# Optimization experiments

Measured on AMD Instinct MI355X. Metric: run time of the kernel, lower is better.

Reference implementation:

```python
import jax, jax.numpy as jnp
import numpy as np

N, E, L = 50000, 800000, 200000
IN_FEATS, HID = 256, 128
EPS = 1e-5


def setup_inputs() -> dict:
    key = jax.random.key(0)
    ks = jax.random.split(key, 32)
    def lin(k, fan_in, fan_out):
        s = 1.0 / np.sqrt(fan_in)
        return jax.random.uniform(k, (fan_out, fan_in), jnp.float32, -s, s)
    inp = {
        "x": jax.random.normal(ks[0], (N, IN_FEATS), jnp.float32),
        "edge_index": jax.random.randint(ks[1], (2, E), 0, N, jnp.int32),
        "edge_label_index": jax.random.randint(ks[2], (2, L), 0, N, jnp.int32),
        # SAGEConv layers: lin_l (on aggregated neighbors, with bias), lin_r (root, no bias)
        "w1l": lin(ks[3], IN_FEATS, HID), "b1l": jnp.zeros((HID,), jnp.float32), "w1r": lin(ks[4], IN_FEATS, HID),
        "w2l": lin(ks[5], HID, HID), "b2l": jnp.zeros((HID,), jnp.float32), "w2r": lin(ks[6], HID, HID),
        "w3l": lin(ks[7], HID, HID), "b3l": jnp.zeros((HID,), jnp.float32), "w3r": lin(ks[8], HID, HID),
        # BatchNorm (eval mode: running stats)
        "bn1_g": jnp.ones((HID,), jnp.float32), "bn1_b": jnp.zeros((HID,), jnp.float32),
        "bn1_m": 0.1 * jax.random.normal(ks[9], (HID,), jnp.float32),
        "bn1_v": jax.random.uniform(ks[10], (HID,), jnp.float32, 0.5, 1.5),
        "bn2_g": jnp.ones((HID,), jnp.float32), "bn2_b": jnp.zeros((HID,), jnp.float32),
        "bn2_m": 0.1 * jax.random.normal(ks[11], (HID,), jnp.float32),
        "bn2_v": jax.random.uniform(ks[12], (HID,), jnp.float32, 0.5, 1.5),
        # Decoder MLP
        "dw1": lin(ks[13], 2 * HID, HID), "db1": jnp.zeros((HID,), jnp.float32),
        "dw2": lin(ks[14], HID, 1), "db2": jnp.zeros((1,), jnp.float32),
    }
    return inp


def _sage_conv(x, src, dst, wl, bl, wr):
    # mean-aggregate neighbor features at dst, then lin_l(agg) + lin_r(x)
    n = x.shape[0]
    agg = jax.ops.segment_sum(x[src], dst, num_segments=n)
    cnt = jax.ops.segment_sum(jnp.ones_like(dst, dtype=x.dtype), dst, num_segments=n)
    mean = agg / jnp.maximum(cnt, 1.0)[:, None]
    return mean @ wl.T + bl + x @ wr.T


def _bn_eval(h, g, b, m, v):
    return (h - m) * (g * jax.lax.rsqrt(v + EPS)) + b


def reference(x, edge_index, edge_label_index,
              w1l, b1l, w1r, w2l, b2l, w2r, w3l, b3l, w3r,
              bn1_g, bn1_b, bn1_m, bn1_v, bn2_g, bn2_b, bn2_m, bn2_v,
              dw1, db1, dw2, db2):
    src, dst = edge_index[0], edge_index[1]
    h = _sage_conv(x, src, dst, w1l, b1l, w1r)
    h = jax.nn.relu(_bn_eval(h, bn1_g, bn1_b, bn1_m, bn1_v))
    h = _sage_conv(h, src, dst, w2l, b2l, w2r)
    h = jax.nn.relu(_bn_eval(h, bn2_g, bn2_b, bn2_m, bn2_v))
    z = _sage_conv(h, src, dst, w3l, b3l, w3r)
    # decode: gather pair embeddings, concat, MLP -> scalar per pair
    s, d = edge_label_index[0], edge_label_index[1]
    pair = jnp.concatenate([z[s], z[d]], axis=1)  # [L, 2*HID]
    hdec = jax.nn.relu(pair @ dw1.T + db1)
    return (hdec @ dw2.T + db2).reshape(-1)
```

## Files before the change

### kernel.cpp

```cpp
#include <hip/hip_runtime.h>
#include <hip/hip_fp16.h>


typedef unsigned int uint;
using s16x8 = __attribute__((ext_vector_type(8))) short;
using f32x4 = __attribute__((ext_vector_type(4))) float;

__device__ inline void bsplit(float v, ushort& hi, ushort& lo) {
    uint u = __float_as_uint(v);
    uint hb = (u + 0x7FFFu + ((u >> 16) & 1u)) >> 16;
    hi = (ushort)hb;
    float r = v - __uint_as_float(hb << 16);
    uint u2 = __float_as_uint(r);
    lo = (ushort)((u2 + 0x7FFFu + ((u2 >> 16) & 1u)) >> 16);
}

__device__ inline ushort f2h(float v) { return __half_as_ushort(__float2half(v)); }

__device__ inline float4 h4f(uint2 r) {
    float2 fa = __half22float2(*(const __half2*)&r.x);
    float2 fb = __half22float2(*(const __half2*)&r.y);
    return make_float4(fa.x, fa.y, fb.x, fb.y);
}

__device__ inline uint swz(uint i, uint r) {
    return (i & ~63u) | ((i ^ (r << 3)) & 56u) | (i & 7u);
}

__device__ inline void gload16(const void* g, void* l) {
    __builtin_amdgcn_global_load_lds(
        (const __attribute__((address_space(1))) unsigned int*)g,
        (__attribute__((address_space(3))) unsigned int*)l, 16, 0, 0);
}

__global__ __launch_bounds__(256) void prep_kernel(
    const float* __restrict__ x, ushort* __restrict__ A3, int totalconv, int nconv,
    const int* __restrict__ dst, int* __restrict__ cnt, int* __restrict__ rank,
    int E, int ncount,
    const float* __restrict__ w1l, const float* __restrict__ w1r,
    const float* __restrict__ w2l, const float* __restrict__ w2r,
    const float* __restrict__ w3l, const float* __restrict__ w3r,
    const float* __restrict__ dw1,
    ushort* __restrict__ WS1, ushort* __restrict__ WS2,
    ushort* __restrict__ WS3, ushort* __restrict__ WS4)
{
    const int g = blockIdx.x >> 4;
    const int r16 = blockIdx.x & 15;
    if (r16 < 12) {
        int ci = g * 12 + r16;
        if (ci >= nconv) return;
        int e = ci * 256 + threadIdx.x;
        if (e >= totalconv) return;
        uint row = e >> 6;
        uint k4 = (e & 63) << 2;
        float4 v = *(const float4*)(x + (size_t)row * 256 + k4);
        ushort4 hi, lo;
        bsplit(v.x, hi.x, lo.x); bsplit(v.y, hi.y, lo.y);
        bsplit(v.z, hi.z, lo.z); bsplit(v.w, hi.w, lo.w);
        ushort* d = A3 + (size_t)row * 512;
        *(ushort4*)(d + swz(k4, row))       = hi;
        *(ushort4*)(d + swz(k4 + 256, row)) = lo;
    } else if (r16 < 15) {
        int qi = g * 3 + (r16 - 12);
        if (qi >= ncount) return;
        int i = qi * 256 + threadIdx.x;
        if (i < E) rank[i] = atomicAdd(&cnt[dst[i]], 1);
    } else {
        int w = g;
        if (w >= 1024) return;
        uint n = w & 255;
        int which = w >> 8;
        uint k = threadIdx.x;
        const float *wa, *wb;
        uint K, lda, aoff, boff;
        ushort* WS;
        switch (which) {
            case 0:  wa = w1l; wb = w1r; K = 256; lda = 256; aoff = 0; boff = 0;   WS = WS1; break;
            case 1:  wa = w2l; wb = w2r; K = 128; lda = 128; aoff = 0; boff = 0;   WS = WS2; break;
            case 2:  wa = w3l; wb = w3r; K = 128; lda = 128; aoff = 0; boff = 0;   WS = WS3; break;
            default: wa = dw1; wb = dw1; K = 128; lda = 256; aoff = 0; boff = 128; WS = WS4; break;
        }
        if (k >= K) return;
        const float* srcr = (n < 128) ? (wa + (size_t)n * lda + aoff)
                                      : (wb + (size_t)(n - 128) * lda + boff);
        ushort hi, lo;
        bsplit(srcr[k], hi, lo);
        ushort* d = WS + (size_t)n * 3 * K;
        d[swz(k, n)]         = hi;
        d[swz(K + k, n)]     = lo;
        d[swz(2 * K + k, n)] = hi;
    }
}

__global__ void scanA_kernel(const int* __restrict__ cnt, int* __restrict__ ptr,
                             int* __restrict__ tilesum, int n) {
    __shared__ int sd[1024];
    int t = threadIdx.x;
    int i = blockIdx.x * 1024 + t;
    int v = (i < n) ? cnt[i] : 0;
    sd[t] = v;
    __syncthreads();
    #pragma unroll
    for (int off = 1; off < 1024; off <<= 1) {
        int add = (t >= off) ? sd[t - off] : 0;
        __syncthreads();
        sd[t] += add;
        __syncthreads();
    }
    if (i < n) ptr[i] = sd[t] - v;
    if (t == 1023) tilesum[blockIdx.x] = sd[t];
}

__global__ void scanC_kernel(int* __restrict__ ptr, const int* __restrict__ tilesum,
                             int n, int ntiles) {
    int i = blockIdx.x * 256 + threadIdx.x;
    int t = i >> 10;
    int base = 0;
    for (int b = 0; b < t; ++b) base += tilesum[b];
    if (i < n) ptr[i] += base;
    if (i == 0) {
        int tot = 0;
        for (int b = 0; b < ntiles; ++b) tot += tilesum[b];
        ptr[n] = tot;
    }
}

__global__ void scatter_kernel(const int* __restrict__ src, const int* __restrict__ dst,
                               const int* __restrict__ ptr, const int* __restrict__ rank,
                               int* __restrict__ edges, int E) {
    int i = blockIdx.x * blockDim.x + threadIdx.x;
    if (i < E) edges[ptr[dst[i]] + rank[i]] = src[i];
}

template <int KP, int CRF16>
__global__ __launch_bounds__(256, 2) void mm_kernel(const ushort* __restrict__ A,
                                                    const ushort* __restrict__ WS,
                                                    ushort* __restrict__ Cl,
                                                    void* __restrict__ Cr_, int M) {
    constexpr int KS  = (KP / 64) + (KP / 128);
    constexpr int WKP = KP + KP / 2;
    __shared__ ushort At[128 * 64];
    __shared__ ushort Bt[256 * 64];
    const int t = threadIdx.x;
    const int lane = t & 63;
    const int wave = t >> 6;
    const int wm = wave >> 1, wn = wave & 1;
    const int row0 = blockIdx.x * 128;
    const int l15 = lane & 15;
    const int l4 = lane >> 4;
    const int l8 = lane >> 3;
    const int c8 = lane & 7;

    f32x4 acc[4][8] = {};

    for (int s = 0; s < KS; ++s) {
        const int as = (s < KP / 128) ? s : s - (KP / 128);
        #pragma unroll
        for (int j = 0; j < 4; ++j) {
            int jj = wave + j * 4;
            int r = jj * 8 + l8;
            gload16(A + (size_t)(row0 + r) * KP + as * 64 + c8 * 8,
                    (char*)At + jj * 1024 + lane * 16);
        }
        #pragma unroll
        for (int j = 0; j < 8; ++j) {
            int jj = wave + j * 4;
            int r = jj * 8 + l8;
            gload16(WS + (size_t)r * WKP + s * 64 + c8 * 8,
                    (char*)Bt + jj * 1024 + lane * 16);
        }
        __syncthreads();
        #pragma unroll
        for (int kk = 0; kk < 64; kk += 32) {
            s16x8 af[4], bf[8];
            #pragma unroll
            for (int mi = 0; mi < 4; ++mi) {
                int r = wm * 64 + mi * 16 + l15;
                int off = (kk + l4 * 8) ^ ((r & 7) * 8);
                af[mi] = *(const s16x8*)&At[r * 64 + off];
            }
            #pragma unroll
            for (int ni = 0; ni < 8; ++ni) {
                int r = wn * 128 + ni * 16 + l15;
                int off = (kk + l4 * 8) ^ ((r & 7) * 8);
                bf[ni] = *(const s16x8*)&Bt[r * 64 + off];
            }
            #pragma unroll
            for (int mi = 0; mi < 4; ++mi)
                #pragma unroll
                for (int ni = 0; ni < 8; ++ni)
                    acc[mi][ni] = __builtin_amdgcn_mfma_f32_16x16x32_bf16(
                        af[mi], bf[ni], acc[mi][ni], 0, 0, 0);
        }
        __syncthreads();
    }
    #pragma unroll
    for (int mi = 0; mi < 4; ++mi) {
        int rbase = row0 + wm * 64 + mi * 16 + l4 * 4;
        #pragma unroll
        for (int ni = 0; ni < 8; ++ni) {
            int col = ni * 16 + l15;
            #pragma unroll
            for (int j = 0; j < 4; ++j) {
                int r = rbase + j;
                if (r < M) {
                    if (wn == 0) {
                        Cl[(size_t)r * 128 + col] = f2h(acc[mi][ni][j]);
                    } else if (CRF16) {
                        ((ushort*)Cr_)[(size_t)r * 128 + col] = f2h(acc[mi][ni][j]);
                    } else {
                        ((float*)Cr_)[(size_t)r * 128 + col] = acc[mi][ni][j];
                    }
                }
            }
        }
    }
}

__global__ __launch_bounds__(256, 4) void agg_kernel(
    const ushort* __restrict__ tl, const float* __restrict__ tr,
    const int* __restrict__ ptr, const int* __restrict__ edges,
    const float* __restrict__ bl,
    const float* __restrict__ bng, const float* __restrict__ bnb,
    const float* __restrict__ bnm, const float* __restrict__ bnv,
    int do_bn, ushort* __restrict__ h3, int n) {
    const int wave = threadIdx.x >> 6;
    const int lane = threadIdx.x & 63;
    const uint node = blockIdx.x * 4 + wave;
    if (node >= (uint)n) return;
    const int half = lane >> 5;
    const uint q4 = (lane & 31) << 2;
    const int p0 = ptr[node], p1 = ptr[node + 1];
    float4 a0 = make_float4(0.f, 0.f, 0.f, 0.f), a1 = a0, a2 = a0, a3 = a0;
    float4 a4 = a0, a5 = a0, a6 = a0, a7 = a0;
    int e = p0 + half;
    int i0 = 0, i1 = 0, i2 = 0, i3 = 0, i4 = 0, i5 = 0, i6 = 0, i7 = 0;
    bool have = (e + 14 < p1);
    if (have) {
        i0 = edges[e];      i1 = edges[e + 2];  i2 = edges[e + 4];  i3 = edges[e + 6];
        i4 = edges[e + 8];  i5 = edges[e + 10]; i6 = edges[e + 12]; i7 = edges[e + 14];
    }
    while (have) {
        int c0 = i0, c1 = i1, c2 = i2, c3 = i3, c4 = i4, c5 = i5, c6 = i6, c7 = i7;
        e += 16;
        have = (e + 14 < p1);
        if (have) {
            i0 = edges[e];      i1 = edges[e + 2];  i2 = edges[e + 4];  i3 = edges[e + 6];
            i4 = edges[e + 8];  i5 = edges[e + 10]; i6 = edges[e + 12]; i7 = edges[e + 14];
        }
        uint2 r0 = *(const uint2*)(tl + (size_t)c0 * 128 + q4);
        uint2 r1 = *(const uint2*)(tl + (size_t)c1 * 128 + q4);
        uint2 r2 = *(const uint2*)(tl + (size_t)c2 * 128 + q4);
        uint2 r3 = *(const uint2*)(tl + (size_t)c3 * 128 + q4);
        uint2 r4 = *(const uint2*)(tl + (size_t)c4 * 128 + q4);
        uint2 r5 = *(const uint2*)(tl + (size_t)c5 * 128 + q4);
        uint2 r6 = *(const uint2*)(tl + (size_t)c6 * 128 + q4);
        uint2 r7 = *(const uint2*)(tl + (size_t)c7 * 128 + q4);
        float4 v0 = h4f(r0), v1 = h4f(r1), v2 = h4f(r2), v3 = h4f(r3);
        float4 v4 = h4f(r4), v5 = h4f(r5), v6 = h4f(r6), v7 = h4f(r7);
        a0.x += v0.x; a0.y += v0.y; a0.z += v0.z; a0.w += v0.w;
        a1.x += v1.x; a1.y += v1.y; a1.z += v1.z; a1.w += v1.w;
        a2.x += v2.x; a2.y += v2.y; a2.z += v2.z; a2.w += v2.w;
        a3.x += v3.x; a3.y += v3.y; a3.z += v3.z; a3.w += v3.w;
        a4.x += v4.x; a4.y += v4.y; a4.z += v4.z; a4.w += v4.w;
        a5.x += v5.x; a5.y += v5.y; a5.z += v5.z; a5.w += v5.w;
        a6.x += v6.x; a6.y += v6.y; a6.z += v6.z; a6.w += v6.w;
        a7.x += v7.x; a7.y += v7.y; a7.z += v7.z; a7.w += v7.w;
    }
    for (; e + 2 < p1; e += 4) {
        int c0 = edges[e], c1 = edges[e + 2];
        float4 v0 = h4f(*(const uint2*)(tl + (size_t)c0 * 128 + q4));
        float4 v1 = h4f(*(const uint2*)(tl + (size_t)c1 * 128 + q4));
        a0.x += v0.x; a0.y += v0.y; a0.z += v0.z; a0.w += v0.w;
        a1.x += v1.x; a1.y += v1.y; a1.z += v1.z; a1.w += v1.w;
    }
    if (e < p1) {
        int c0 = edges[e];
        float4 v0 = h4f(*(const uint2*)(tl + (size_t)c0 * 128 + q4));
        a2.x += v0.x; a2.y += v0.y; a2.z += v0.z; a2.w += v0.w;
    }
    float4 s;
    s.x = ((a0.x + a1.x) + (a2.x + a3.x)) + ((a4.x + a5.x) + (a6.x + a7.x));
    s.y = ((a0.y + a1.y) + (a2.y + a3.y)) + ((a4.y + a5.y) + (a6.y + a7.y));
    s.z = ((a0.z + a1.z) + (a2.z + a3.z)) + ((a4.z + a5.z) + (a6.z + a7.z));
    s.w = ((a0.w + a1.w) + (a2.w + a3.w)) + ((a4.w + a5.w) + (a6.w + a7.w));
    s.x += __shfl_xor(s.x, 32);
    s.y += __shfl_xor(s.y, 32);
    s.z += __shfl_xor(s.z, 32);
    s.w += __shfl_xor(s.w, 32);
    if (half == 0) {
        float inv = 1.f / fmaxf((float)(p1 - p0), 1.f);
        float4 r = *(const float4*)(tr + (size_t)node * 128 + q4);
        float4 b = *(const float4*)(bl + q4);
        float4 val;
        val.x = fmaf(s.x, inv, b.x) + r.x;
        val.y = fmaf(s.y, inv, b.y) + r.y;
        val.z = fmaf(s.z, inv, b.z) + r.z;
        val.w = fmaf(s.w, inv, b.w) + r.w;
        if (do_bn) {
            float4 g = *(const float4*)(bng + q4);
            float4 be = *(const float4*)(bnb + q4);
            float4 m = *(const float4*)(bnm + q4);
            float4 vv = *(const float4*)(bnv + q4);
            val.x = fmaxf(fmaf(val.x - m.x, g.x * rsqrtf(vv.x + 1e-5f), be.x), 0.f);
            val.y = fmaxf(fmaf(val.y - m.y, g.y * rsqrtf(vv.y + 1e-5f), be.y), 0.f);
            val.z = fmaxf(fmaf(val.z - m.z, g.z * rsqrtf(vv.z + 1e-5f), be.z), 0.f);
            val.w = fmaxf(fmaf(val.w - m.w, g.w * rsqrtf(vv.w + 1e-5f), be.w), 0.f);
        }
        ushort4 hi, lo;
        bsplit(val.x, hi.x, lo.x); bsplit(val.y, hi.y, lo.y);
        bsplit(val.z, hi.z, lo.z); bsplit(val.w, hi.w, lo.w);
        ushort* d = h3 + (size_t)node * 256;
        *(ushort4*)(d + swz(q4, node))       = hi;
        *(ushort4*)(d + swz(q4 + 128, node)) = lo;
    }
}

__global__ __launch_bounds__(256) void decode_kernel(
    const ushort* __restrict__ u, const ushort* __restrict__ v,
    const int* __restrict__ eli, const float* __restrict__ db1,
    const float* __restrict__ dw2, const float* __restrict__ db2,
    float* __restrict__ out, int L) {
    __shared__ float sb[128], sw[128];
    if (threadIdx.x < 128) {
        sb[threadIdx.x] = db1[threadIdx.x];
        sw[threadIdx.x] = dw2[threadIdx.x];
    }
    __syncthreads();
    int p = blockIdx.x * 256 + threadIdx.x;
    if (p >= L) return;
    int s = eli[p], d = eli[L + p];
    const ushort* up = u + (size_t)s * 128;
    const ushort* vp = v + (size_t)d * 128;
    float acc = db2[0];
    #pragma unroll 8
    for (int o = 0; o < 128; o += 4) {
        float4 a = h4f(*(const uint2*)(up + o));
        float4 b = h4f(*(const uint2*)(vp + o));
        float4 bb = *(const float4*)(&sb[o]);
        float4 w = *(const float4*)(&sw[o]);
        acc += fmaxf(a.x + b.x + bb.x, 0.f) * w.x;
        acc += fmaxf(a.y + b.y + bb.y, 0.f) * w.y;
        acc += fmaxf(a.z + b.z + bb.z, 0.f) * w.z;
        acc += fmaxf(a.w + b.w + bb.w, 0.f) * w.w;
    }
    out[p] = acc;
}

extern "C" void kernel_launch(void* const* d_in, const int* in_sizes, int n_in,
                              void* d_out, int out_size, void* d_ws, size_t ws_size,
                              hipStream_t stream) {
    const float* x    = (const float*)d_in[0];
    const int*   ei   = (const int*)d_in[1];
    const int*   eli  = (const int*)d_in[2];
    const float* w1l  = (const float*)d_in[3];
    const float* b1l  = (const float*)d_in[4];
    const float* w1r  = (const float*)d_in[5];
    const float* w2l  = (const float*)d_in[6];
    const float* b2l  = (const float*)d_in[7];
    const float* w2r  = (const float*)d_in[8];
    const float* w3l  = (const float*)d_in[9];
    const float* b3l  = (const float*)d_in[10];
    const float* w3r  = (const float*)d_in[11];
    const float* bn1g = (const float*)d_in[12];
    const float* bn1b = (const float*)d_in[13];
    const float* bn1m = (const float*)d_in[14];
    const float* bn1v = (const float*)d_in[15];
    const float* bn2g = (const float*)d_in[16];
    const float* bn2b = (const float*)d_in[17];
    const float* bn2m = (const float*)d_in[18];
    const float* bn2v = (const float*)d_in[19];
    const float* dw1  = (const float*)d_in[20];
    const float* db1  = (const float*)d_in[21];
    const float* dw2  = (const float*)d_in[22];
    const float* db2  = (const float*)d_in[23];
    float* out = (float*)d_out;

    const int N = in_sizes[0] / 256;
    const int E = in_sizes[1] / 2;
    const int L = in_sizes[2] / 2;
    const int* src = ei;
    const int* dst = ei + E;
    const int ntiles = (N + 1023) >> 10;
    const int nblk = (N + 127) / 128;
    const int Npad = nblk * 128;
    const int nconv = (N * 64 + 255) / 256;
    const int ncount = (E + 255) / 256;
    int G16 = (nconv + 11) / 12;
    if ((ncount + 2) / 3 > G16) G16 = (ncount + 2) / 3;
    if (1024 > G16) G16 = 1024;

    char* wsb = (char*)d_ws;
    size_t off = 0;
    auto carve = [&](size_t bytes) -> void* {
        void* p = wsb + off;
        off += (bytes + 255) & ~(size_t)255;
        return p;
    };
    int* ptr        = (int*)carve((size_t)(N + 1) * 4);
    int* cnt        = (int*)carve((size_t)N * 4);
    int* rank       = (int*)carve((size_t)E * 4);
    int* tilesum    = (int*)carve((size_t)ntiles * 4);
    int* edges      = (int*)carve((size_t)E * 4);
    ushort* WS1     = (ushort*)carve((size_t)256 * 768 * 2);
    ushort* WS2     = (ushort*)carve((size_t)256 * 384 * 2);
    ushort* WS3     = (ushort*)carve((size_t)256 * 384 * 2);
    ushort* WS4     = (ushort*)carve((size_t)256 * 384 * 2);
    ushort* tl_h    = (ushort*)carve((size_t)N * 128 * 2);
    float* tr_c     = (float*)carve((size_t)N * 128 * 4);
    ushort* A3      = (ushort*)carve((size_t)Npad * 512 * 2);
    ushort* h3      = A3;

    hipMemsetAsync(cnt, 0, (size_t)N * 4, stream);
    prep_kernel<<<G16 * 16, 256, 0, stream>>>(
        x, A3, N * 64, nconv, dst, cnt, rank, E, ncount,
        w1l, w1r, w2l, w2r, w3l, w3r, dw1, WS1, WS2, WS3, WS4);
    scanA_kernel<<<ntiles, 1024, 0, stream>>>(cnt, ptr, tilesum, N);
    scanC_kernel<<<(N + 255) / 256, 256, 0, stream>>>(ptr, tilesum, N, ntiles);
    scatter_kernel<<<(E + 255) / 256, 256, 0, stream>>>(src, dst, ptr, rank, edges, E);

    mm_kernel<512, 0><<<nblk, 256, 0, stream>>>(A3, WS1, tl_h, tr_c, N);
    agg_kernel<<<(N + 3) / 4, 256, 0, stream>>>(tl_h, tr_c, ptr, edges, b1l,
                                                bn1g, bn1b, bn1m, bn1v, 1, h3, N);
    mm_kernel<256, 0><<<nblk, 256, 0, stream>>>(h3, WS2, tl_h, tr_c, N);
    agg_kernel<<<(N + 3) / 4, 256, 0, stream>>>(tl_h, tr_c, ptr, edges, b2l,
                                                bn2g, bn2b, bn2m, bn2v, 1, h3, N);
    mm_kernel<256, 0><<<nblk, 256, 0, stream>>>(h3, WS3, tl_h, tr_c, N);
    agg_kernel<<<(N + 3) / 4, 256, 0, stream>>>(tl_h, tr_c, ptr, edges, b3l,
                                                bn1g, bn1b, bn1m, bn1v, 0, h3, N);
    mm_kernel<256, 1><<<nblk, 256, 0, stream>>>(h3, WS4, tl_h, tr_c, N);
    decode_kernel<<<(L + 255) / 256, 256, 0, stream>>>(tl_h, (const ushort*)tr_c, eli,
                                                       db1, dw2, db2, out, L);
}
```

Measured before the change: 341.5 us.

## Switch split-precision GEMM from bf16x3 to fp16 hi/lo activations with fp16 weights

Activations are now split into fp16 hi and lo parts, and weights are stored as a single fp16 copy instead of bf16 hi/lo/hi. Each GEMM therefore runs two MFMA passes (A_hi·W + A_lo·W) instead of three, and the weight staging loads shrink to K columns. The f16 MFMA replaces the bf16 one. This removes a third of the matrix work and weight traffic, but weights lose their low-order correction. fp16 also has a narrower range, which may reduce accuracy.

```diff
diff --git a/kernel.cpp b/kernel.cpp
--- a/kernel.cpp
+++ b/kernel.cpp
@@ -3,19 +3,16 @@
 
 
 typedef unsigned int uint;
-using s16x8 = __attribute__((ext_vector_type(8))) short;
+using f16x8 = __attribute__((ext_vector_type(8))) _Float16;
 using f32x4 = __attribute__((ext_vector_type(4))) float;
 
-__device__ inline void bsplit(float v, ushort& hi, ushort& lo) {
-    uint u = __float_as_uint(v);
-    uint hb = (u + 0x7FFFu + ((u >> 16) & 1u)) >> 16;
-    hi = (ushort)hb;
-    float r = v - __uint_as_float(hb << 16);
-    uint u2 = __float_as_uint(r);
-    lo = (ushort)((u2 + 0x7FFFu + ((u2 >> 16) & 1u)) >> 16);
-}
-
 __device__ inline ushort f2h(float v) { return __half_as_ushort(__float2half(v)); }
+
+__device__ inline void fsplit(float v, ushort& hi, ushort& lo) {
+    __half h = __float2half(v);
+    hi = __half_as_ushort(h);
+    lo = __half_as_ushort(__float2half(v - __half2float(h)));
+}
 
 __device__ inline float4 h4f(uint2 r) {
     float2 fa = __half22float2(*(const __half2*)&r.x);
@@ -55,8 +52,8 @@
         uint k4 = (e & 63) << 2;
         float4 v = *(const float4*)(x + (size_t)row * 256 + k4);
         ushort4 hi, lo;
-        bsplit(v.x, hi.x, lo.x); bsplit(v.y, hi.y, lo.y);
-        bsplit(v.z, hi.z, lo.z); bsplit(v.w, hi.w, lo.w);
+        fsplit(v.x, hi.x, lo.x); fsplit(v.y, hi.y, lo.y);
+        fsplit(v.z, hi.z, lo.z); fsplit(v.w, hi.w, lo.w);
         ushort* d = A3 + (size_t)row * 512;
         *(ushort4*)(d + swz(k4, row))       = hi;
         *(ushort4*)(d + swz(k4 + 256, row)) = lo;
@@ -83,12 +80,8 @@
         if (k >= K) return;
         const float* srcr = (n < 128) ? (wa + (size_t)n * lda + aoff)
                                       : (wb + (size_t)(n - 128) * lda + boff);
-        ushort hi, lo;
-        bsplit(srcr[k], hi, lo);
-        ushort* d = WS + (size_t)n * 3 * K;
-        d[swz(k, n)]         = hi;
-        d[swz(K + k, n)]     = lo;
-        d[swz(2 * K + k, n)] = hi;
+        ushort* d = WS + (size_t)n * K;
+        d[swz(k, n)] = f2h(srcr[k]);
     }
 }
 
@@ -132,14 +125,13 @@
     if (i < E) edges[ptr[dst[i]] + rank[i]] = src[i];
 }
 
-template <int KP, int CRF16>
+template <int K, int CRF16>
 __global__ __launch_bounds__(256, 2) void mm_kernel(const ushort* __restrict__ A,
                                                     const ushort* __restrict__ WS,
                                                     ushort* __restrict__ Cl,
                                                     void* __restrict__ Cr_, int M) {
-    constexpr int KS  = (KP / 64) + (KP / 128);
-    constexpr int WKP = KP + KP / 2;
-    __shared__ ushort At[128 * 64];
+    constexpr int KS = K / 64;
+    __shared__ ushort At[2 * 128 * 64];
     __shared__ ushort Bt[256 * 64];
     const int t = threadIdx.x;
     const int lane = t & 63;
@@ -154,43 +146,47 @@
     f32x4 acc[4][8] = {};
 
     for (int s = 0; s < KS; ++s) {
-        const int as = (s < KP / 128) ? s : s - (KP / 128);
         #pragma unroll
         for (int j = 0; j < 4; ++j) {
             int jj = wave + j * 4;
             int r = jj * 8 + l8;
-            gload16(A + (size_t)(row0 + r) * KP + as * 64 + c8 * 8,
-                    (char*)At + jj * 1024 + lane * 16);
+            const ushort* ga = A + (size_t)(row0 + r) * (2 * K) + s * 64 + c8 * 8;
+            gload16(ga,     (char*)At + jj * 1024 + lane * 16);
+            gload16(ga + K, (char*)At + 16384 + jj * 1024 + lane * 16);
         }
         #pragma unroll
         for (int j = 0; j < 8; ++j) {
             int jj = wave + j * 4;
             int r = jj * 8 + l8;
-            gload16(WS + (size_t)r * WKP + s * 64 + c8 * 8,
+            gload16(WS + (size_t)r * K + s * 64 + c8 * 8,
                     (char*)Bt + jj * 1024 + lane * 16);
         }
         __syncthreads();
         #pragma unroll
         for (int kk = 0; kk < 64; kk += 32) {
-            s16x8 af[4], bf[8];
-            #pragma unroll
-            for (int mi = 0; mi < 4; ++mi) {
-                int r = wm * 64 + mi * 16 + l15;
-                int off = (kk + l4 * 8) ^ ((r & 7) * 8);
-                af[mi] = *(const s16x8*)&At[r * 64 + off];
-            }
+            f16x8 bf[8];
             #pragma unroll
             for (int ni = 0; ni < 8; ++ni) {
                 int r = wn * 128 + ni * 16 + l15;
                 int off = (kk + l4 * 8) ^ ((r & 7) * 8);
-                bf[ni] = *(const s16x8*)&Bt[r * 64 + off];
+                bf[ni] = *(const f16x8*)&Bt[r * 64 + off];
             }
             #pragma unroll
-            for (int mi = 0; mi < 4; ++mi)
+            for (int h = 0; h < 2; ++h) {
+                f16x8 af[4];
                 #pragma unroll
-                for (int ni = 0; ni < 8; ++ni)
-                    acc[mi][ni] = __builtin_amdgcn_mfma_f32_16x16x32_bf16(
-                        af[mi], bf[ni], acc[mi][ni], 0, 0, 0);
+                for (int mi = 0; mi < 4; ++mi) {
+                    int r = wm * 64 + mi * 16 + l15;
+                    int off = (kk + l4 * 8) ^ ((r & 7) * 8);
+                    af[mi] = *(const f16x8*)&At[h * 8192 + r * 64 + off];
+                }
+                #pragma unroll
+                for (int mi = 0; mi < 4; ++mi)
+                    #pragma unroll
+                    for (int ni = 0; ni < 8; ++ni)
+                        acc[mi][ni] = __builtin_amdgcn_mfma_f32_16x16x32_f16(
+                            af[mi], bf[ni], acc[mi][ni], 0, 0, 0);
+            }
         }
         __syncthreads();
     }
@@ -308,8 +304,8 @@
             val.w = fmaxf(fmaf(val.w - m.w, g.w * rsqrtf(vv.w + 1e-5f), be.w), 0.f);
         }
         ushort4 hi, lo;
-        bsplit(val.x, hi.x, lo.x); bsplit(val.y, hi.y, lo.y);
-        bsplit(val.z, hi.z, lo.z); bsplit(val.w, hi.w, lo.w);
+        fsplit(val.x, hi.x, lo.x); fsplit(val.y, hi.y, lo.y);
+        fsplit(val.z, hi.z, lo.z); fsplit(val.w, hi.w, lo.w);
         ushort* d = h3 + (size_t)node * 256;
         *(ushort4*)(d + swz(q4, node))       = hi;
         *(ushort4*)(d + swz(q4 + 128, node)) = lo;
@@ -402,10 +398,10 @@
     int* rank       = (int*)carve((size_t)E * 4);
     int* tilesum    = (int*)carve((size_t)ntiles * 4);
     int* edges      = (int*)carve((size_t)E * 4);
-    ushort* WS1     = (ushort*)carve((size_t)256 * 768 * 2);
-    ushort* WS2     = (ushort*)carve((size_t)256 * 384 * 2);
-    ushort* WS3     = (ushort*)carve((size_t)256 * 384 * 2);
-    ushort* WS4     = (ushort*)carve((size_t)256 * 384 * 2);
+    ushort* WS1     = (ushort*)carve((size_t)256 * 256 * 2);
+    ushort* WS2     = (ushort*)carve((size_t)256 * 128 * 2);
+    ushort* WS3     = (ushort*)carve((size_t)256 * 128 * 2);
+    ushort* WS4     = (ushort*)carve((size_t)256 * 128 * 2);
     ushort* tl_h    = (ushort*)carve((size_t)N * 128 * 2);
     float* tr_c     = (float*)carve((size_t)N * 128 * 4);
     ushort* A3      = (ushort*)carve((size_t)Npad * 512 * 2);
@@ -419,16 +415,16 @@
     scanC_kernel<<<(N + 255) / 256, 256, 0, stream>>>(ptr, tilesum, N, ntiles);
     scatter_kernel<<<(E + 255) / 256, 256, 0, stream>>>(src, dst, ptr, rank, edges, E);
 
-    mm_kernel<512, 0><<<nblk, 256, 0, stream>>>(A3, WS1, tl_h, tr_c, N);
+    mm_kernel<256, 0><<<nblk, 256, 0, stream>>>(A3, WS1, tl_h, tr_c, N);
     agg_kernel<<<(N + 3) / 4, 256, 0, stream>>>(tl_h, tr_c, ptr, edges, b1l,
                                                 bn1g, bn1b, bn1m, bn1v, 1, h3, N);
-    mm_kernel<256, 0><<<nblk, 256, 0, stream>>>(h3, WS2, tl_h, tr_c, N);
+    mm_kernel<128, 0><<<nblk, 256, 0, stream>>>(h3, WS2, tl_h, tr_c, N);
     agg_kernel<<<(N + 3) / 4, 256, 0, stream>>>(tl_h, tr_c, ptr, edges, b2l,
                                                 bn2g, bn2b, bn2m, bn2v, 1, h3, N);
-    mm_kernel<256, 0><<<nblk, 256, 0, stream>>>(h3, WS3, tl_h, tr_c, N);
+    mm_kernel<128, 0><<<nblk, 256, 0, stream>>>(h3, WS3, tl_h, tr_c, N);
     agg_kernel<<<(N + 3) / 4, 256, 0, stream>>>(tl_h, tr_c, ptr, edges, b3l,
                                                 bn1g, bn1b, bn1m, bn1v, 0, h3, N);
-    mm_kernel<256, 1><<<nblk, 256, 0, stream>>>(h3, WS4, tl_h, tr_c, N);
+    mm_kernel<128, 1><<<nblk, 256, 0, stream>>>(h3, WS4, tl_h, tr_c, N);
     decode_kernel<<<(L + 255) / 256, 256, 0, stream>>>(tl_h, (const ushort*)tr_c, eli,
                                                        db1, dw2, db2, out, L);
 }
```

After: 314.0 us, median of 2. -8.0%, faster.
